# Performance work log

Hardware: AMD Instinct MI355X
Metric: run time of the kernel (lower is better)

Reference implementation:

```python
import jax, jax.numpy as jnp
import numpy as np

DEPTH = 6
N_INTERNAL = 2 ** DEPTH - 1  # 63
N_LEAVES = 2 ** DEPTH        # 64


def _tree_paths(depth):
    """Precompute, for each leaf, its `depth` ancestor internal-node indices and
    whether the path goes right at each ancestor (static heap-indexing of the tree)."""
    n_internal = 2 ** depth - 1
    n_leaves = 2 ** depth
    anc = np.zeros((n_leaves, depth), dtype=np.int32)
    right = np.zeros((n_leaves, depth), dtype=bool)
    for leaf in range(n_leaves):
        node = leaf + n_internal
        for d in range(depth):
            parent = (node - 1) // 2
            anc[leaf, d] = parent
            right[leaf, d] = (node % 2 == 0)
            node = parent
    return jnp.asarray(anc), jnp.asarray(right)

_ANC, _RIGHT = _tree_paths(DEPTH)


def setup_inputs() -> dict:
    key = jax.random.key(0)
    k = jax.random.split(key, 6)
    B, F, T, C = 8192, 256, 32, 100
    return {
        "x": jax.random.normal(k[0], (B, F), dtype=jnp.float32),
        "split_weights": jax.random.normal(k[1], (T, N_INTERNAL, F), dtype=jnp.float32) * 0.05,
        "split_bias": jax.random.normal(k[2], (T, N_INTERNAL), dtype=jnp.float32) * 0.05,
        "leaf_logits": jax.random.normal(k[3], (T, N_LEAVES, C), dtype=jnp.float32),
        "tree_weights": jax.random.normal(k[4], (T,), dtype=jnp.float32),
        "log_temperature": jnp.zeros((), dtype=jnp.float32),
    }


def reference(x, split_weights, split_bias, leaf_logits, tree_weights, log_temperature):
    # temperature = exp(log_temperature).clamp(0.1, 5.0)
    temp = jnp.clip(jnp.exp(log_temperature), 0.1, 5.0)
    # split probabilities for all trees at once: [T, B, N_INTERNAL]
    logits = jnp.einsum('bf,tnf->tbn', x, split_weights) + split_bias[:, None, :]
    split_probs = jax.nn.sigmoid(logits / temp)
    # gather each leaf's ancestor probs: [T, B, L, D]; right -> p, left -> 1-p
    g = split_probs[:, :, _ANC]
    leaf_probs = jnp.prod(jnp.where(_RIGHT, g, 1.0 - g), axis=-1)  # [T, B, L]
    # per-leaf class distributions: [T, L, C]
    leaf_class_probs = jax.nn.softmax(leaf_logits / temp, axis=-1)
    outputs = jnp.einsum('tbl,tlc->tbc', leaf_probs, leaf_class_probs)  # [T, B, C]
    weights = jax.nn.softmax(tree_weights, axis=0)  # [T]
    return jnp.einsum('t,tbc->bc', weights, outputs)  # [B, C]
```

## Files before the change

kernel.cpp:

```cpp
#include <hip/hip_runtime.h>
#include <math.h>

#define B_  8192
#define F_  256
#define T_  32
#define NI_ 63
#define NL_ 64
#define C_  100
#define K2_ (T_*NL_)
#define NG  4
#define TPG 8

typedef unsigned short u16;
typedef __attribute__((ext_vector_type(8))) short bf16x8;
typedef __attribute__((ext_vector_type(4))) float f32x4;
typedef __attribute__((ext_vector_type(8))) unsigned short u16x8;

__device__ __forceinline__ u16 f2bf(float f) {
    unsigned int u = __float_as_uint(f);
    u += 0x7fffu + ((u >> 16) & 1u);
    return (u16)(u >> 16);
}
__device__ __forceinline__ float bf2f(u16 u) {
    return __uint_as_float(((unsigned int)u) << 16);
}

#define WSB_SWB   0
#define WSB_LCPT  (T_*NI_*F_*2)
#define WSB_PART  ((size_t)WSB_LCPT + 112*K2_*2)
#define WSB_ATOM  WSB_PART
#define WSB_STORE (WSB_PART + (size_t)NG*B_*112*2)

#define SWBLK  (T_*NI_*F_/256)
#define LCPBLK (T_*NL_/256)
#define ZBLK   (B_*C_/256)
__global__ void k_prep(const float* __restrict__ sw, const float* __restrict__ ll,
                       const float* __restrict__ tw, const float* __restrict__ logT,
                       u16* __restrict__ swb, u16* __restrict__ lcpT,
                       float* __restrict__ out) {
    int blk = blockIdx.x, tid = threadIdx.x;
    if (blk < SWBLK) { int i = blk * 256 + tid; swb[i] = f2bf(sw[i]); return; }
    blk -= SWBLK;
    if (blk >= LCPBLK) {
        out[(blk - LCPBLK) * 256 + tid] = 0.f;
        return;
    }
    int idx = blk * 256 + tid;
    int t = idx >> 6;
    float temp = __expf(logT[0]);
    temp = fminf(fmaxf(temp, 0.1f), 5.0f);
    float invt = 1.0f / temp;

    float m = -1e30f;
    for (int j = 0; j < T_; ++j) m = fmaxf(m, tw[j]);
    float s = 0.f;
    for (int j = 0; j < T_; ++j) s += __expf(tw[j] - m);
    float wt = __expf(tw[t] - m) / s;

    const float* row = ll + (size_t)idx * C_;
    float m2 = -1e30f;
    for (int c = 0; c < C_; ++c) m2 = fmaxf(m2, row[c]);
    float s2 = 0.f;
    for (int c = 0; c < C_; ++c) s2 += __expf((row[c] - m2) * invt);
    float sc = wt / s2;
    for (int c = 0; c < C_; ++c)
        lcpT[(size_t)c * K2_ + idx] = f2bf(sc * __expf((row[c] - m2) * invt));
    for (int c = C_; c < 112; ++c)
        lcpT[(size_t)c * K2_ + idx] = 0;
}

__global__ __launch_bounds__(256, 2)
void k_fused(const float* __restrict__ x, const u16* __restrict__ swb,
             const float* __restrict__ sb, const float* __restrict__ logT,
             const u16* __restrict__ lcpT, void* __restrict__ dst, int storeMode) {
    __shared__ u16   swS[63 * 264];
    __shared__ u16   lcpS[8 * 112 * 8];
    __shared__ float slog[4][16][66];
    int tid  = threadIdx.x;
    int w    = tid >> 6;
    int lane = tid & 63;
    int col  = lane & 15;
    int quad = lane >> 4;
    int mb   = blockIdx.x * 64 + w * 16;
    int tg   = blockIdx.y;

    float temp = __expf(logT[0]);
    temp = fminf(fmaxf(temp, 0.1f), 5.0f);
    float invt = 1.0f / temp;

    bf16x8 afr[8];
    #pragma unroll
    for (int ks = 0; ks < 8; ++ks) {
        const float4* px = (const float4*)(x + (size_t)(mb + col) * F_ + ks * 32 + quad * 8);
        float4 v0 = px[0], v1 = px[1];
        bf16x8 a;
        a[0] = (short)f2bf(v0.x); a[1] = (short)f2bf(v0.y);
        a[2] = (short)f2bf(v0.z); a[3] = (short)f2bf(v0.w);
        a[4] = (short)f2bf(v1.x); a[5] = (short)f2bf(v1.y);
        a[6] = (short)f2bf(v1.z); a[7] = (short)f2bf(v1.w);
        afr[ks] = a;
    }

    u16x8 pf_sw[8];
    u16x8 pf_lcp[4];
    {
        int t0 = tg * TPG;
        const char* gsrc = (const char*)(swb + (size_t)t0 * NI_ * F_);
        #pragma unroll
        for (int r = 0; r < 8; ++r) {
            int g = r * 4096 + tid * 16;
            if (g < NI_ * F_ * 2) pf_sw[r] = *(const u16x8*)(gsrc + g);
        }
        #pragma unroll
        for (int r = 0; r < 4; ++r) {
            int idx = r * 256 + tid;
            if (idx < 896) {
                int o = idx / 112, c = idx - o * 112;
                pf_lcp[r] = *(const u16x8*)(lcpT + (size_t)c * K2_ + t0 * NL_ + o * 8);
            }
        }
    }

    f32x4 accO[7];
    #pragma unroll
    for (int i = 0; i < 7; ++i) accO[i] = (f32x4){0.f, 0.f, 0.f, 0.f};

    #pragma unroll 1
    for (int ti = 0; ti < TPG; ++ti) {
        int t = tg * TPG + ti;

        __syncthreads();
        #pragma unroll
        for (int r = 0; r < 8; ++r) {
            int g = r * 4096 + tid * 16;
            if (g < NI_ * F_ * 2) {
                int n   = g >> 9;
                int k16 = (g & 511) >> 4;
                *(u16x8*)&swS[n * 264 + k16 * 8] = pf_sw[r];
            }
        }
        #pragma unroll
        for (int r = 0; r < 4; ++r) {
            int idx = r * 256 + tid;
            if (idx < 896) {
                int o = idx / 112, c = idx - o * 112;
                *(u16x8*)&lcpS[(o * 112 + c) * 8] = pf_lcp[r];
            }
        }
        __syncthreads();

        if (ti + 1 < TPG) {
            int tn = t + 1;
            const char* gsrc = (const char*)(swb + (size_t)tn * NI_ * F_);
            #pragma unroll
            for (int r = 0; r < 8; ++r) {
                int g = r * 4096 + tid * 16;
                if (g < NI_ * F_ * 2) pf_sw[r] = *(const u16x8*)(gsrc + g);
            }
            #pragma unroll
            for (int r = 0; r < 4; ++r) {
                int idx = r * 256 + tid;
                if (idx < 896) {
                    int o = idx / 112, c = idx - o * 112;
                    pf_lcp[r] = *(const u16x8*)(lcpT + (size_t)c * K2_ + tn * NL_ + o * 8);
                }
            }
        }

        f32x4 acc[4];
        #pragma unroll
        for (int i = 0; i < 4; ++i) acc[i] = (f32x4){0.f, 0.f, 0.f, 0.f};
        #pragma unroll
        for (int ks = 0; ks < 8; ++ks) {
            #pragma unroll
            for (int nt = 0; nt < 4; ++nt) {
                int n  = nt * 16 + col;
                int ne = n > 62 ? 62 : n;
                bf16x8 bfr = *(const bf16x8*)&swS[ne * 264 + ks * 32 + quad * 8];
                acc[nt] = __builtin_amdgcn_mfma_f32_16x16x32_bf16(afr[ks], bfr, acc[nt], 0, 0, 0);
            }
        }

        asm volatile("s_waitcnt lgkmcnt(0)" ::: "memory");
        #pragma unroll
        for (int nt = 0; nt < 4; ++nt) {
            int n = nt * 16 + col;
            float bias = (n < NI_) ? sb[t * NI_ + n] : 0.f;
            #pragma unroll
            for (int r = 0; r < 4; ++r) {
                float lg = (acc[nt][r] + bias) * invt;
                slog[w][quad * 4 + r][n] = 1.0f / (1.0f + __expf(-lg));
            }
        }
        asm volatile("s_waitcnt lgkmcnt(0)" ::: "memory");

        bf16x8 af0, af1;
        #pragma unroll
        for (int grp = 0; grp < 2; ++grp) {
            int s = (grp ? 11 : 7) + quad;
            float pref = 1.0f;
            int node = s;
            #pragma unroll
            for (int d = 0; d < 3; ++d) {
                int par = (node - 1) >> 1;
                float g = slog[w][col][par];
                pref = (node & 1) ? (pref - pref * g) : (pref * g);
                node = par;
            }
            float gs  = slog[w][col][s];
            float gl  = slog[w][col][2 * s + 1];
            float gr  = slog[w][col][2 * s + 2];
            float g00 = slog[w][col][4 * s + 3];
            float g01 = slog[w][col][4 * s + 4];
            float g10 = slog[w][col][4 * s + 5];
            float g11 = slog[w][col][4 * s + 6];
            #pragma unroll
            for (int j = 0; j < 8; ++j) {
                const int b2 = (j >> 2) & 1, b1 = (j >> 1) & 1, b0 = j & 1;
                float f3 = b2 ? gs : 1.0f - gs;
                float c1 = b2 ? gr : gl;
                float f4 = b1 ? c1 : 1.0f - c1;
                float c2 = b2 ? (b1 ? g11 : g10) : (b1 ? g01 : g00);
                float f5 = b0 ? c2 : 1.0f - c2;
                float p  = pref * f3 * f4 * f5;
                if (grp == 0) af0[j] = (short)f2bf(p);
                else          af1[j] = (short)f2bf(p);
            }
        }

        #pragma unroll
        for (int nt = 0; nt < 7; ++nt) {
            int n = nt * 16 + col;
            bf16x8 lb0 = *(const bf16x8*)&lcpS[(quad * 112 + n) * 8];
            bf16x8 lb1 = *(const bf16x8*)&lcpS[((4 + quad) * 112 + n) * 8];
            accO[nt] = __builtin_amdgcn_mfma_f32_16x16x32_bf16(af0, lb0, accO[nt], 0, 0, 0);
            accO[nt] = __builtin_amdgcn_mfma_f32_16x16x32_bf16(af1, lb1, accO[nt], 0, 0, 0);
        }
    }

    if (storeMode) {
        u16* pp = (u16*)dst + (size_t)tg * B_ * 112;
        #pragma unroll
        for (int nt = 0; nt < 7; ++nt) {
            int c = nt * 16 + col;
            #pragma unroll
            for (int r = 0; r < 4; ++r) {
                int b = mb + quad * 4 + r;
                pp[(size_t)b * 112 + c] = f2bf(accO[nt][r]);
            }
        }
    } else {
        float* od = (float*)dst;
        #pragma unroll
        for (int nt = 0; nt < 7; ++nt) {
            int c = nt * 16 + col;
            if (c < C_) {
                #pragma unroll
                for (int r = 0; r < 4; ++r) {
                    int b = mb + quad * 4 + r;
                    atomicAdd(&od[(size_t)b * C_ + c], accO[nt][r]);
                }
            }
        }
    }
}

__global__ void k_red(const u16* __restrict__ part, float* __restrict__ out) {
    int idx = blockIdx.x * 256 + threadIdx.x;
    int b = idx / 112, c = idx - b * 112;
    if (c < C_) {
        float s = 0.f;
        #pragma unroll
        for (int tg = 0; tg < NG; ++tg)
            s += bf2f(part[((size_t)tg * B_ + b) * 112 + c]);
        out[(size_t)b * C_ + c] = s;
    }
}

__global__ void k_zf(float* __restrict__ out, int n) {
    int i = blockIdx.x * 256 + threadIdx.x;
    if (i < n) out[i] = 0.f;
}

__global__ void k_mono(const float* __restrict__ x, const float* __restrict__ sw,
                       const float* __restrict__ sb, const float* __restrict__ ll,
                       const float* __restrict__ tw, const float* __restrict__ logT,
                       float* __restrict__ outg) {
    __shared__ float slcp[NL_ * C_];
    int tid = threadIdx.x;
    int b = blockIdx.x * 256 + tid;

    float temp = __expf(logT[0]);
    temp = fminf(fmaxf(temp, 0.1f), 5.0f);
    float invt = 1.0f / temp;

    float m = -1e30f;
    for (int j = 0; j < T_; ++j) m = fmaxf(m, tw[j]);
    float sden = 0.f;
    for (int j = 0; j < T_; ++j) sden += __expf(tw[j] - m);

    float acc[C_];
    #pragma unroll
    for (int c = 0; c < C_; ++c) acc[c] = 0.f;

    for (int t = 0; t < T_; ++t) {
        __syncthreads();
        {
            int l = tid & 63, cq = tid >> 6;
            float wt = __expf(tw[t] - m) / sden;
            const float* row = ll + ((size_t)t * NL_ + l) * C_;
            float m2 = -1e30f;
            for (int c = 0; c < C_; ++c) m2 = fmaxf(m2, row[c]);
            float s2 = 0.f;
            for (int c = 0; c < C_; ++c) s2 += __expf((row[c] - m2) * invt);
            float sc = wt / s2;
            for (int c = cq * 25; c < cq * 25 + 25; ++c)
                slcp[l * C_ + c] = sc * __expf((row[c] - m2) * invt);
        }
        __syncthreads();

        float an[NI_];
        #pragma unroll
        for (int n = 0; n < NI_; ++n) an[n] = 0.f;
        for (int k = 0; k < F_; ++k) {
            float xv = x[(size_t)b * F_ + k];
            #pragma unroll
            for (int n = 0; n < NI_; ++n)
                an[n] = fmaf(xv, sw[((size_t)t * NI_ + n) * F_ + k], an[n]);
        }
        #pragma unroll
        for (int n = 0; n < NI_; ++n) {
            float lg = (an[n] + sb[t * NI_ + n]) * invt;
            an[n] = 1.0f / (1.0f + __expf(-lg));
        }
        #pragma unroll
        for (int l = 0; l < NL_; ++l) {
            int node = l + NI_;
            float p = 1.0f;
            #pragma unroll
            for (int d = 0; d < 6; ++d) {
                int par = (node - 1) >> 1;
                float gv = an[par];
                p = (node & 1) ? (p - p * gv) : (p * gv);
                node = par;
            }
            #pragma unroll
            for (int c = 0; c < C_; ++c)
                acc[c] = fmaf(p, slcp[l * C_ + c], acc[c]);
        }
    }
    for (int c = 0; c < C_; ++c)
        outg[(size_t)b * C_ + c] = acc[c];
}

extern "C" void kernel_launch(void* const* d_in, const int* in_sizes, int n_in,
                              void* d_out, int out_size, void* d_ws, size_t ws_size,
                              hipStream_t stream) {
    bool ok = (n_in >= 6)
           && (in_sizes[0] == B_ * F_)
           && (in_sizes[1] == T_ * NI_ * F_)
           && (in_sizes[2] == T_ * NI_)
           && (in_sizes[3] == T_ * NL_ * C_)
           && (in_sizes[4] == T_)
           && (in_sizes[5] == 1)
           && (out_size == B_ * C_);
    if (!ok) {
        k_zf<<<(out_size + 255) / 256, 256, 0, stream>>>((float*)d_out, out_size);
        return;
    }

    const float* x    = (const float*)d_in[0];
    const float* sw   = (const float*)d_in[1];
    const float* sb   = (const float*)d_in[2];
    const float* ll   = (const float*)d_in[3];
    const float* tw   = (const float*)d_in[4];
    const float* logT = (const float*)d_in[5];
    float* out = (float*)d_out;

    if (ws_size >= WSB_STORE) {
        u16* swb  = (u16*)((char*)d_ws + WSB_SWB);
        u16* lcpT = (u16*)((char*)d_ws + WSB_LCPT);
        u16* part = (u16*)((char*)d_ws + WSB_PART);

        k_prep <<<SWBLK + LCPBLK, 256, 0, stream>>>(sw, ll, tw, logT, swb, lcpT, out);
        k_fused<<<dim3(B_ / 64, NG), 256, 0, stream>>>(x, swb, sb, logT, lcpT, part, 1);
        k_red  <<<(B_ * 112) / 256, 256, 0, stream>>>(part, out);
    } else if (ws_size >= WSB_ATOM) {
        u16* swb  = (u16*)((char*)d_ws + WSB_SWB);
        u16* lcpT = (u16*)((char*)d_ws + WSB_LCPT);

        k_prep <<<SWBLK + LCPBLK + ZBLK, 256, 0, stream>>>(sw, ll, tw, logT, swb, lcpT, out);
        k_fused<<<dim3(B_ / 64, NG), 256, 0, stream>>>(x, swb, sb, logT, lcpT, d_out, 0);
    } else {
        k_mono<<<B_ / 256, 256, 0, stream>>>(x, sw, sb, ll, tw, logT, out);
    }
}
```

Measured before the change: 129.2 us.

## Double per-wave batch rows and pre-convert x to bf16 in prep kernel

Each wave now handles 32 batch rows instead of 16, so every split-weight and leaf-prob fragment read from LDS feeds two MFMAs. The tree dimension is re-split into 8 groups of 4 trees, which restores grid parallelism at 64x8 blocks. x is converted to bf16 once in the prep kernel, and the sw conversion is vectorized to 8 elements per thread, so the fused kernel reads bf16 directly. In exchange the kernel holds more accumulator and fragment registers, which may hurt occupancy, the partial-sum buffer and reduction double in size, and there is an extra workspace pass over x.

```diff
diff --git a/kernel.cpp b/kernel.cpp
--- a/kernel.cpp
+++ b/kernel.cpp
@@ -8,8 +8,8 @@
 #define NL_ 64
 #define C_  100
 #define K2_ (T_*NL_)
-#define NG  4
-#define TPG 8
+#define NG  8
+#define TPG 4
 
 typedef unsigned short u16;
 typedef __attribute__((ext_vector_type(8))) short bf16x8;
@@ -27,20 +27,35 @@
 
 #define WSB_SWB   0
 #define WSB_LCPT  (T_*NI_*F_*2)
-#define WSB_PART  ((size_t)WSB_LCPT + 112*K2_*2)
+#define WSB_XB    (WSB_LCPT + 112*K2_*2)
+#define WSB_PART  ((size_t)WSB_XB + (size_t)B_*F_*2)
 #define WSB_ATOM  WSB_PART
 #define WSB_STORE (WSB_PART + (size_t)NG*B_*112*2)
 
-#define SWBLK  (T_*NI_*F_/256)
+#define SWBLK  (T_*NI_*F_/2048)
+#define XBLK   (B_*F_/2048)
 #define LCPBLK (T_*NL_/256)
 #define ZBLK   (B_*C_/256)
-__global__ void k_prep(const float* __restrict__ sw, const float* __restrict__ ll,
-                       const float* __restrict__ tw, const float* __restrict__ logT,
-                       u16* __restrict__ swb, u16* __restrict__ lcpT,
-                       float* __restrict__ out) {
+
+__device__ __forceinline__ void cvt8(const float* __restrict__ s, u16* __restrict__ d, int i) {
+    const float4* p = (const float4*)(s + i);
+    float4 v0 = p[0], v1 = p[1];
+    u16x8 o;
+    o[0] = f2bf(v0.x); o[1] = f2bf(v0.y); o[2] = f2bf(v0.z); o[3] = f2bf(v0.w);
+    o[4] = f2bf(v1.x); o[5] = f2bf(v1.y); o[6] = f2bf(v1.z); o[7] = f2bf(v1.w);
+    *(u16x8*)(d + i) = o;
+}
+
+__global__ void k_prep(const float* __restrict__ sw, const float* __restrict__ x,
+                       const float* __restrict__ ll, const float* __restrict__ tw,
+                       const float* __restrict__ logT,
+                       u16* __restrict__ swb, u16* __restrict__ xb,
+                       u16* __restrict__ lcpT, float* __restrict__ out) {
     int blk = blockIdx.x, tid = threadIdx.x;
-    if (blk < SWBLK) { int i = blk * 256 + tid; swb[i] = f2bf(sw[i]); return; }
+    if (blk < SWBLK) { cvt8(sw, swb, blk * 2048 + tid * 8); return; }
     blk -= SWBLK;
+    if (blk < XBLK) { cvt8(x, xb, blk * 2048 + tid * 8); return; }
+    blk -= XBLK;
     if (blk >= LCPBLK) {
         out[(blk - LCPBLK) * 256 + tid] = 0.f;
         return;
@@ -70,36 +85,30 @@
 }
 
 __global__ __launch_bounds__(256, 2)
-void k_fused(const float* __restrict__ x, const u16* __restrict__ swb,
+void k_fused(const u16* __restrict__ xb, const u16* __restrict__ swb,
              const float* __restrict__ sb, const float* __restrict__ logT,
              const u16* __restrict__ lcpT, void* __restrict__ dst, int storeMode) {
-    __shared__ u16   swS[63 * 264];
-    __shared__ u16   lcpS[8 * 112 * 8];
-    __shared__ float slog[4][16][66];
+    __shared__ __attribute__((aligned(16))) u16 swS[63 * 264];
+    __shared__ __attribute__((aligned(16))) u16 lcpS[8 * 112 * 8];
+    __shared__ float slog[4][32][66];
     int tid  = threadIdx.x;
     int w    = tid >> 6;
     int lane = tid & 63;
     int col  = lane & 15;
     int quad = lane >> 4;
-    int mb   = blockIdx.x * 64 + w * 16;
+    int mb   = blockIdx.x * 128 + w * 32;
     int tg   = blockIdx.y;
 
     float temp = __expf(logT[0]);
     temp = fminf(fmaxf(temp, 0.1f), 5.0f);
     float invt = 1.0f / temp;
 
-    bf16x8 afr[8];
+    bf16x8 afr[2][8];
     #pragma unroll
-    for (int ks = 0; ks < 8; ++ks) {
-        const float4* px = (const float4*)(x + (size_t)(mb + col) * F_ + ks * 32 + quad * 8);
-        float4 v0 = px[0], v1 = px[1];
-        bf16x8 a;
-        a[0] = (short)f2bf(v0.x); a[1] = (short)f2bf(v0.y);
-        a[2] = (short)f2bf(v0.z); a[3] = (short)f2bf(v0.w);
-        a[4] = (short)f2bf(v1.x); a[5] = (short)f2bf(v1.y);
-        a[6] = (short)f2bf(v1.z); a[7] = (short)f2bf(v1.w);
-        afr[ks] = a;
-    }
+    for (int rs = 0; rs < 2; ++rs)
+        #pragma unroll
+        for (int ks = 0; ks < 8; ++ks)
+            afr[rs][ks] = *(const bf16x8*)(xb + (size_t)(mb + rs * 16 + col) * F_ + ks * 32 + quad * 8);
 
     u16x8 pf_sw[8];
     u16x8 pf_lcp[4];
@@ -121,9 +130,11 @@
         }
     }
 
-    f32x4 accO[7];
+    f32x4 accO[2][7];
     #pragma unroll
-    for (int i = 0; i < 7; ++i) accO[i] = (f32x4){0.f, 0.f, 0.f, 0.f};
+    for (int rs = 0; rs < 2; ++rs)
+        #pragma unroll
+        for (int i = 0; i < 7; ++i) accO[rs][i] = (f32x4){0.f, 0.f, 0.f, 0.f};
 
     #pragma unroll 1
     for (int ti = 0; ti < TPG; ++ti) {
@@ -167,9 +178,11 @@
             }
         }
 
-        f32x4 acc[4];
-        #pragma unroll
-        for (int i = 0; i < 4; ++i) acc[i] = (f32x4){0.f, 0.f, 0.f, 0.f};
+        f32x4 acc[2][4];
+        #pragma unroll
+        for (int rs = 0; rs < 2; ++rs)
+            #pragma unroll
+            for (int i = 0; i < 4; ++i) acc[rs][i] = (f32x4){0.f, 0.f, 0.f, 0.f};
         #pragma unroll
         for (int ks = 0; ks < 8; ++ks) {
             #pragma unroll
@@ -177,7 +190,8 @@
                 int n  = nt * 16 + col;
                 int ne = n > 62 ? 62 : n;
                 bf16x8 bfr = *(const bf16x8*)&swS[ne * 264 + ks * 32 + quad * 8];
-                acc[nt] = __builtin_amdgcn_mfma_f32_16x16x32_bf16(afr[ks], bfr, acc[nt], 0, 0, 0);
+                acc[0][nt] = __builtin_amdgcn_mfma_f32_16x16x32_bf16(afr[0][ks], bfr, acc[0][nt], 0, 0, 0);
+                acc[1][nt] = __builtin_amdgcn_mfma_f32_16x16x32_bf16(afr[1][ks], bfr, acc[1][nt], 0, 0, 0);
             }
         }
 
@@ -187,44 +201,50 @@
             int n = nt * 16 + col;
             float bias = (n < NI_) ? sb[t * NI_ + n] : 0.f;
             #pragma unroll
-            for (int r = 0; r < 4; ++r) {
-                float lg = (acc[nt][r] + bias) * invt;
-                slog[w][quad * 4 + r][n] = 1.0f / (1.0f + __expf(-lg));
+            for (int rs = 0; rs < 2; ++rs) {
+                #pragma unroll
+                for (int r = 0; r < 4; ++r) {
+                    float lg = (acc[rs][nt][r] + bias) * invt;
+                    slog[w][rs * 16 + quad * 4 + r][n] = 1.0f / (1.0f + __expf(-lg));
+                }
             }
         }
         asm volatile("s_waitcnt lgkmcnt(0)" ::: "memory");
 
-        bf16x8 af0, af1;
-        #pragma unroll
-        for (int grp = 0; grp < 2; ++grp) {
-            int s = (grp ? 11 : 7) + quad;
-            float pref = 1.0f;
-            int node = s;
-            #pragma unroll
-            for (int d = 0; d < 3; ++d) {
-                int par = (node - 1) >> 1;
-                float g = slog[w][col][par];
-                pref = (node & 1) ? (pref - pref * g) : (pref * g);
-                node = par;
-            }
-            float gs  = slog[w][col][s];
-            float gl  = slog[w][col][2 * s + 1];
-            float gr  = slog[w][col][2 * s + 2];
-            float g00 = slog[w][col][4 * s + 3];
-            float g01 = slog[w][col][4 * s + 4];
-            float g10 = slog[w][col][4 * s + 5];
-            float g11 = slog[w][col][4 * s + 6];
-            #pragma unroll
-            for (int j = 0; j < 8; ++j) {
-                const int b2 = (j >> 2) & 1, b1 = (j >> 1) & 1, b0 = j & 1;
-                float f3 = b2 ? gs : 1.0f - gs;
-                float c1 = b2 ? gr : gl;
-                float f4 = b1 ? c1 : 1.0f - c1;
-                float c2 = b2 ? (b1 ? g11 : g10) : (b1 ? g01 : g00);
-                float f5 = b0 ? c2 : 1.0f - c2;
-                float p  = pref * f3 * f4 * f5;
-                if (grp == 0) af0[j] = (short)f2bf(p);
-                else          af1[j] = (short)f2bf(p);
+        bf16x8 af[2][2];
+        #pragma unroll
+        for (int rs = 0; rs < 2; ++rs) {
+            const float* sl = &slog[w][rs * 16 + col][0];
+            #pragma unroll
+            for (int grp = 0; grp < 2; ++grp) {
+                int s = (grp ? 11 : 7) + quad;
+                float pref = 1.0f;
+                int node = s;
+                #pragma unroll
+                for (int d = 0; d < 3; ++d) {
+                    int par = (node - 1) >> 1;
+                    float g = sl[par];
+                    pref = (node & 1) ? (pref - pref * g) : (pref * g);
+                    node = par;
+                }
+                float gs  = sl[s];
+                float gl  = sl[2 * s + 1];
+                float gr  = sl[2 * s + 2];
+                float g00 = sl[4 * s + 3];
+                float g01 = sl[4 * s + 4];
+                float g10 = sl[4 * s + 5];
+                float g11 = sl[4 * s + 6];
+                #pragma unroll
+                for (int j = 0; j < 8; ++j) {
+                    const int b2 = (j >> 2) & 1, b1 = (j >> 1) & 1, b0 = j & 1;
+                    float f3 = b2 ? gs : 1.0f - gs;
+                    float c1 = b2 ? gr : gl;
+                    float f4 = b1 ? c1 : 1.0f - c1;
+                    float c2 = b2 ? (b1 ? g11 : g10) : (b1 ? g01 : g00);
+                    float f5 = b0 ? c2 : 1.0f - c2;
+                    float p  = pref * f3 * f4 * f5;
+                    af[rs][grp][j] = (short)f2bf(p);
+                }
             }
         }
 
@@ -233,8 +253,10 @@
             int n = nt * 16 + col;
             bf16x8 lb0 = *(const bf16x8*)&lcpS[(quad * 112 + n) * 8];
             bf16x8 lb1 = *(const bf16x8*)&lcpS[((4 + quad) * 112 + n) * 8];
-            accO[nt] = __builtin_amdgcn_mfma_f32_16x16x32_bf16(af0, lb0, accO[nt], 0, 0, 0);
-            accO[nt] = __builtin_amdgcn_mfma_f32_16x16x32_bf16(af1, lb1, accO[nt], 0, 0, 0);
+            accO[0][nt] = __builtin_amdgcn_mfma_f32_16x16x32_bf16(af[0][0], lb0, accO[0][nt], 0, 0, 0);
+            accO[0][nt] = __builtin_amdgcn_mfma_f32_16x16x32_bf16(af[0][1], lb1, accO[0][nt], 0, 0, 0);
+            accO[1][nt] = __builtin_amdgcn_mfma_f32_16x16x32_bf16(af[1][0], lb0, accO[1][nt], 0, 0, 0);
+            accO[1][nt] = __builtin_amdgcn_mfma_f32_16x16x32_bf16(af[1][1], lb1, accO[1][nt], 0, 0, 0);
         }
     }
 
@@ -244,9 +266,12 @@
         for (int nt = 0; nt < 7; ++nt) {
             int c = nt * 16 + col;
             #pragma unroll
-            for (int r = 0; r < 4; ++r) {
-                int b = mb + quad * 4 + r;
-                pp[(size_t)b * 112 + c] = f2bf(accO[nt][r]);
+            for (int rs = 0; rs < 2; ++rs) {
+                #pragma unroll
+                for (int r = 0; r < 4; ++r) {
+                    int b = mb + rs * 16 + quad * 4 + r;
+                    pp[(size_t)b * 112 + c] = f2bf(accO[rs][nt][r]);
+                }
             }
         }
     } else {
@@ -256,9 +281,12 @@
             int c = nt * 16 + col;
             if (c < C_) {
                 #pragma unroll
-                for (int r = 0; r < 4; ++r) {
-                    int b = mb + quad * 4 + r;
-                    atomicAdd(&od[(size_t)b * C_ + c], accO[nt][r]);
+                for (int rs = 0; rs < 2; ++rs) {
+                    #pragma unroll
+                    for (int r = 0; r < 4; ++r) {
+                        int b = mb + rs * 16 + quad * 4 + r;
+                        atomicAdd(&od[(size_t)b * C_ + c], accO[rs][nt][r]);
+                    }
                 }
             }
         }
@@ -380,17 +408,19 @@
     if (ws_size >= WSB_STORE) {
         u16* swb  = (u16*)((char*)d_ws + WSB_SWB);
         u16* lcpT = (u16*)((char*)d_ws + WSB_LCPT);
+        u16* xb   = (u16*)((char*)d_ws + WSB_XB);
         u16* part = (u16*)((char*)d_ws + WSB_PART);
 
-        k_prep <<<SWBLK + LCPBLK, 256, 0, stream>>>(sw, ll, tw, logT, swb, lcpT, out);
-        k_fused<<<dim3(B_ / 64, NG), 256, 0, stream>>>(x, swb, sb, logT, lcpT, part, 1);
+        k_prep <<<SWBLK + XBLK + LCPBLK, 256, 0, stream>>>(sw, x, ll, tw, logT, swb, xb, lcpT, out);
+        k_fused<<<dim3(B_ / 128, NG), 256, 0, stream>>>(xb, swb, sb, logT, lcpT, part, 1);
         k_red  <<<(B_ * 112) / 256, 256, 0, stream>>>(part, out);
     } else if (ws_size >= WSB_ATOM) {
         u16* swb  = (u16*)((char*)d_ws + WSB_SWB);
         u16* lcpT = (u16*)((char*)d_ws + WSB_LCPT);
-
-        k_prep <<<SWBLK + LCPBLK + ZBLK, 256, 0, stream>>>(sw, ll, tw, logT, swb, lcpT, out);
-        k_fused<<<dim3(B_ / 64, NG), 256, 0, stream>>>(x, swb, sb, logT, lcpT, d_out, 0);
+        u16* xb   = (u16*)((char*)d_ws + WSB_XB);
+
+        k_prep <<<SWBLK + XBLK + LCPBLK + ZBLK, 256, 0, stream>>>(sw, x, ll, tw, logT, swb, xb, lcpT, out);
+        k_fused<<<dim3(B_ / 128, NG), 256, 0, stream>>>(xb, swb, sb, logT, lcpT, d_out, 0);
     } else {
         k_mono<<<B_ / 256, 256, 0, stream>>>(x, sw, sb, ll, tw, logT, out);
     }
```

After: 137.7 us. 6.6% more time.

## Pre-convert x to bf16 and widen fused blocks to 128 rows across 8 tree groups

Applied to the files above, without the earlier changes.

The prep kernel now also converts x to bf16 into workspace, and both conversions handle eight elements per thread with vector loads and stores. The fused kernel loads A fragments directly as bf16, which removes the per-block fp32 conversion. It also runs 512 threads (8 waves, 128 rows) per block, so each staged tree's split weights and leaf probabilities serve twice as many rows. Trees are split into 8 groups of 4 instead of 4 groups of 8, which adds parallelism but doubles the partial-sum traffic in the reduction and grows the workspace needed.

```diff
diff --git a/kernel.cpp b/kernel.cpp
--- a/kernel.cpp
+++ b/kernel.cpp
@@ -8,8 +8,8 @@
 #define NL_ 64
 #define C_  100
 #define K2_ (T_*NL_)
-#define NG  4
-#define TPG 8
+#define NG  8
+#define TPG 4
 
 typedef unsigned short u16;
 typedef __attribute__((ext_vector_type(8))) short bf16x8;
@@ -27,20 +27,35 @@
 
 #define WSB_SWB   0
 #define WSB_LCPT  (T_*NI_*F_*2)
-#define WSB_PART  ((size_t)WSB_LCPT + 112*K2_*2)
+#define WSB_XB    (WSB_LCPT + 112*K2_*2)
+#define WSB_PART  ((size_t)WSB_XB + (size_t)B_*F_*2)
 #define WSB_ATOM  WSB_PART
 #define WSB_STORE (WSB_PART + (size_t)NG*B_*112*2)
 
-#define SWBLK  (T_*NI_*F_/256)
+#define SWBLK  (T_*NI_*F_/2048)
+#define XBLK   (B_*F_/2048)
 #define LCPBLK (T_*NL_/256)
 #define ZBLK   (B_*C_/256)
-__global__ void k_prep(const float* __restrict__ sw, const float* __restrict__ ll,
-                       const float* __restrict__ tw, const float* __restrict__ logT,
-                       u16* __restrict__ swb, u16* __restrict__ lcpT,
-                       float* __restrict__ out) {
+
+__device__ __forceinline__ void cvt8(const float* __restrict__ s, u16* __restrict__ d, int i) {
+    const float4* p = (const float4*)(s + i);
+    float4 v0 = p[0], v1 = p[1];
+    u16x8 o;
+    o[0] = f2bf(v0.x); o[1] = f2bf(v0.y); o[2] = f2bf(v0.z); o[3] = f2bf(v0.w);
+    o[4] = f2bf(v1.x); o[5] = f2bf(v1.y); o[6] = f2bf(v1.z); o[7] = f2bf(v1.w);
+    *(u16x8*)(d + i) = o;
+}
+
+__global__ void k_prep(const float* __restrict__ sw, const float* __restrict__ x,
+                       const float* __restrict__ ll, const float* __restrict__ tw,
+                       const float* __restrict__ logT,
+                       u16* __restrict__ swb, u16* __restrict__ xb,
+                       u16* __restrict__ lcpT, float* __restrict__ out) {
     int blk = blockIdx.x, tid = threadIdx.x;
-    if (blk < SWBLK) { int i = blk * 256 + tid; swb[i] = f2bf(sw[i]); return; }
+    if (blk < SWBLK) { cvt8(sw, swb, blk * 2048 + tid * 8); return; }
     blk -= SWBLK;
+    if (blk < XBLK) { cvt8(x, xb, blk * 2048 + tid * 8); return; }
+    blk -= XBLK;
     if (blk >= LCPBLK) {
         out[(blk - LCPBLK) * 256 + tid] = 0.f;
         return;
@@ -69,19 +84,19 @@
         lcpT[(size_t)c * K2_ + idx] = 0;
 }
 
-__global__ __launch_bounds__(256, 2)
-void k_fused(const float* __restrict__ x, const u16* __restrict__ swb,
+__global__ __launch_bounds__(512, 4)
+void k_fused(const u16* __restrict__ xb, const u16* __restrict__ swb,
              const float* __restrict__ sb, const float* __restrict__ logT,
              const u16* __restrict__ lcpT, void* __restrict__ dst, int storeMode) {
-    __shared__ u16   swS[63 * 264];
-    __shared__ u16   lcpS[8 * 112 * 8];
-    __shared__ float slog[4][16][66];
+    __shared__ __attribute__((aligned(16))) u16 swS[63 * 264];
+    __shared__ __attribute__((aligned(16))) u16 lcpS[8 * 112 * 8];
+    __shared__ float slog[8][16][66];
     int tid  = threadIdx.x;
     int w    = tid >> 6;
     int lane = tid & 63;
     int col  = lane & 15;
     int quad = lane >> 4;
-    int mb   = blockIdx.x * 64 + w * 16;
+    int mb   = blockIdx.x * 128 + w * 16;
     int tg   = blockIdx.y;
 
     float temp = __expf(logT[0]);
@@ -90,30 +105,22 @@
 
     bf16x8 afr[8];
     #pragma unroll
-    for (int ks = 0; ks < 8; ++ks) {
-        const float4* px = (const float4*)(x + (size_t)(mb + col) * F_ + ks * 32 + quad * 8);
-        float4 v0 = px[0], v1 = px[1];
-        bf16x8 a;
-        a[0] = (short)f2bf(v0.x); a[1] = (short)f2bf(v0.y);
-        a[2] = (short)f2bf(v0.z); a[3] = (short)f2bf(v0.w);
-        a[4] = (short)f2bf(v1.x); a[5] = (short)f2bf(v1.y);
-        a[6] = (short)f2bf(v1.z); a[7] = (short)f2bf(v1.w);
-        afr[ks] = a;
-    }
-
-    u16x8 pf_sw[8];
-    u16x8 pf_lcp[4];
+    for (int ks = 0; ks < 8; ++ks)
+        afr[ks] = *(const bf16x8*)(xb + (size_t)(mb + col) * F_ + ks * 32 + quad * 8);
+
+    u16x8 pf_sw[4];
+    u16x8 pf_lcp[2];
     {
         int t0 = tg * TPG;
         const char* gsrc = (const char*)(swb + (size_t)t0 * NI_ * F_);
         #pragma unroll
-        for (int r = 0; r < 8; ++r) {
-            int g = r * 4096 + tid * 16;
+        for (int r = 0; r < 4; ++r) {
+            int g = r * 8192 + tid * 16;
             if (g < NI_ * F_ * 2) pf_sw[r] = *(const u16x8*)(gsrc + g);
         }
         #pragma unroll
-        for (int r = 0; r < 4; ++r) {
-            int idx = r * 256 + tid;
+        for (int r = 0; r < 2; ++r) {
+            int idx = r * 512 + tid;
             if (idx < 896) {
                 int o = idx / 112, c = idx - o * 112;
                 pf_lcp[r] = *(const u16x8*)(lcpT + (size_t)c * K2_ + t0 * NL_ + o * 8);
@@ -131,8 +138,8 @@
 
         __syncthreads();
         #pragma unroll
-        for (int r = 0; r < 8; ++r) {
-            int g = r * 4096 + tid * 16;
+        for (int r = 0; r < 4; ++r) {
+            int g = r * 8192 + tid * 16;
             if (g < NI_ * F_ * 2) {
                 int n   = g >> 9;
                 int k16 = (g & 511) >> 4;
@@ -140,8 +147,8 @@
             }
         }
         #pragma unroll
-        for (int r = 0; r < 4; ++r) {
-            int idx = r * 256 + tid;
+        for (int r = 0; r < 2; ++r) {
+            int idx = r * 512 + tid;
             if (idx < 896) {
                 int o = idx / 112, c = idx - o * 112;
                 *(u16x8*)&lcpS[(o * 112 + c) * 8] = pf_lcp[r];
@@ -153,13 +160,13 @@
             int tn = t + 1;
             const char* gsrc = (const char*)(swb + (size_t)tn * NI_ * F_);
             #pragma unroll
-            for (int r = 0; r < 8; ++r) {
-                int g = r * 4096 + tid * 16;
+            for (int r = 0; r < 4; ++r) {
+                int g = r * 8192 + tid * 16;
                 if (g < NI_ * F_ * 2) pf_sw[r] = *(const u16x8*)(gsrc + g);
             }
             #pragma unroll
-            for (int r = 0; r < 4; ++r) {
-                int idx = r * 256 + tid;
+            for (int r = 0; r < 2; ++r) {
+                int idx = r * 512 + tid;
                 if (idx < 896) {
                     int o = idx / 112, c = idx - o * 112;
                     pf_lcp[r] = *(const u16x8*)(lcpT + (size_t)c * K2_ + tn * NL_ + o * 8);
@@ -380,17 +387,19 @@
     if (ws_size >= WSB_STORE) {
         u16* swb  = (u16*)((char*)d_ws + WSB_SWB);
         u16* lcpT = (u16*)((char*)d_ws + WSB_LCPT);
+        u16* xb   = (u16*)((char*)d_ws + WSB_XB);
         u16* part = (u16*)((char*)d_ws + WSB_PART);
 
-        k_prep <<<SWBLK + LCPBLK, 256, 0, stream>>>(sw, ll, tw, logT, swb, lcpT, out);
-        k_fused<<<dim3(B_ / 64, NG), 256, 0, stream>>>(x, swb, sb, logT, lcpT, part, 1);
+        k_prep <<<SWBLK + XBLK + LCPBLK, 256, 0, stream>>>(sw, x, ll, tw, logT, swb, xb, lcpT, out);
+        k_fused<<<dim3(B_ / 128, NG), 512, 0, stream>>>(xb, swb, sb, logT, lcpT, part, 1);
         k_red  <<<(B_ * 112) / 256, 256, 0, stream>>>(part, out);
     } else if (ws_size >= WSB_ATOM) {
         u16* swb  = (u16*)((char*)d_ws + WSB_SWB);
         u16* lcpT = (u16*)((char*)d_ws + WSB_LCPT);
-
-        k_prep <<<SWBLK + LCPBLK + ZBLK, 256, 0, stream>>>(sw, ll, tw, logT, swb, lcpT, out);
-        k_fused<<<dim3(B_ / 64, NG), 256, 0, stream>>>(x, swb, sb, logT, lcpT, d_out, 0);
+        u16* xb   = (u16*)((char*)d_ws + WSB_XB);
+
+        k_prep <<<SWBLK + XBLK + LCPBLK + ZBLK, 256, 0, stream>>>(sw, x, ll, tw, logT, swb, xb, lcpT, out);
+        k_fused<<<dim3(B_ / 128, NG), 512, 0, stream>>>(xb, swb, sb, logT, lcpT, d_out, 0);
     } else {
         k_mono<<<B_ / 256, 256, 0, stream>>>(x, sw, sb, ll, tw, logT, out);
     }
```

Measured after the change: 145.7 us. +12.8%, slower.
